# Kernel tuning notes

Measured on AMD Instinct MI355X. Metric: run time of the kernel, lower is better.

The kernel has to match this reference:

```python
import jax, jax.numpy as jnp
import numpy as np

N = 100000
E = 3200000
IN_FEATS = 128
HID_FEATS = 128
OUT_FEATS = 128
MLP_HID = 128
MLP_OUT = 64


def setup_inputs() -> dict:
    key = jax.random.key(0)
    ks = jax.random.split(key, 12)
    x = jax.random.normal(ks[0], (N, IN_FEATS), dtype=jnp.float32)
    src = jax.random.randint(ks[1], (E,), 0, N, dtype=jnp.int32)
    dst = jax.random.randint(ks[2], (E,), 0, N, dtype=jnp.int32)
    s = 0.05
    W1 = jax.random.normal(ks[3], (IN_FEATS, HID_FEATS), dtype=jnp.float32) * s
    b1 = jnp.zeros((HID_FEATS,), dtype=jnp.float32)
    W2 = jax.random.normal(ks[4], (HID_FEATS, OUT_FEATS), dtype=jnp.float32) * s
    b2 = jnp.zeros((OUT_FEATS,), dtype=jnp.float32)
    Wm1 = jax.random.normal(ks[5], (OUT_FEATS, MLP_HID), dtype=jnp.float32) * s
    bm1 = jnp.zeros((MLP_HID,), dtype=jnp.float32)
    Wm2 = jax.random.normal(ks[6], (MLP_HID, MLP_OUT), dtype=jnp.float32) * s
    bm2 = jnp.zeros((MLP_OUT,), dtype=jnp.float32)
    return {"x": x, "src": src, "dst": dst, "W1": W1, "b1": b1,
            "W2": W2, "b2": b2, "Wm1": Wm1, "bm1": bm1, "Wm2": Wm2, "bm2": bm2}


def _graph_conv(h, src, dst, W, b, out_norm, in_norm):
    # DGL GraphConv norm='both': rst = D_in^{-1/2} * A^T (D_out^{-1/2} * h) @ W + b
    msg = (h * out_norm[:, None])[src]                       # [E, F] gather
    agg = jax.ops.segment_sum(msg, dst, num_segments=N)      # [N, F] scatter-add
    return (agg * in_norm[:, None]) @ W + b


def _forward(x, src, dst, W1, b1, W2, b2, Wm1, bm1, Wm2, bm2):
    ones = jnp.ones((src.shape[0],), dtype=x.dtype)
    out_deg = jnp.maximum(jax.ops.segment_sum(ones, src, num_segments=N), 1.0)
    in_deg = jnp.maximum(jax.ops.segment_sum(ones, dst, num_segments=N), 1.0)
    out_norm = out_deg ** -0.5
    in_norm = in_deg ** -0.5
    # conv1 + ReLU (dropout identity in eval mode)
    h = jax.nn.relu(_graph_conv(x, src, dst, W1, b1, out_norm, in_norm))
    # conv2 + ReLU
    h = jax.nn.relu(_graph_conv(h, src, dst, W2, b2, out_norm, in_norm))
    # MLP head: Linear -> ReLU -> Linear -> sigmoid (act='sigmoid')
    h = jax.nn.relu(h @ Wm1 + bm1)
    h = jax.nn.sigmoid(h @ Wm2 + bm2)
    return h


def reference(x, src, dst, W1, b1, W2, b2, Wm1, bm1, Wm2, bm2):
    return _forward(x, src, dst, W1, b1, W2, b2, Wm1, bm1, Wm2, bm2)
```

## Files before the change

### kernel.cpp

```cpp
#include <hip/hip_runtime.h>
#include <math.h>

#define NNODES 100000
#define NEDGES 3200000
#define F 128
#define NPB 512
#define NB ((NNODES + NPB - 1) / NPB)
#define CAP 20480
#define T2 8192

typedef __attribute__((ext_vector_type(8))) short short8;
typedef __attribute__((ext_vector_type(4))) float f32x4;

__device__ __forceinline__ unsigned short f2bf(float f) {
    unsigned u = __float_as_uint(f);
    unsigned r = u + 0x7fff + ((u >> 16) & 1);
    return (unsigned short)(r >> 16);
}
__device__ __forceinline__ float bflo(unsigned u) { return __uint_as_float(u << 16); }
__device__ __forceinline__ float bfhi(unsigned u) { return __uint_as_float(u & 0xffff0000u); }


__global__ void init_cursors_kernel(int* __restrict__ dcur, int* __restrict__ scur) {
    int b = blockIdx.x * 256 + threadIdx.x;
    if (b < NB) { dcur[b] = b * CAP; scur[b] = b * CAP; }
}


__global__ __launch_bounds__(256) void dual_bin_kernel(const int* __restrict__ src,
                                                       const int* __restrict__ dst,
                                                       int* __restrict__ dcur,
                                                       int* __restrict__ scur,
                                                       unsigned* __restrict__ epk,
                                                       unsigned short* __restrict__ esl) {
    __shared__ unsigned pk[T2];
    __shared__ unsigned short sl[T2];
    __shared__ unsigned char db[T2], sb[T2];
    __shared__ int dh[NB], dbase[NB], dlc[NB];
    __shared__ int sh[NB], sbase[NB], slc[NB];
    int t = threadIdx.x;
    for (int i = t; i < NB; i += 256) { dh[i] = 0; dlc[i] = 0; sh[i] = 0; slc[i] = 0; }
    __syncthreads();
    int e0 = blockIdx.x * T2;
    int n = min(T2, NEDGES - e0);
    for (int i = t; i < n; i += 256) {
        int s = src[e0 + i], d = dst[e0 + i];
        int bd = d >> 9, bs = s >> 9;
        pk[i] = (unsigned)s | ((unsigned)(d & 511) << 17);
        sl[i] = (unsigned short)(s & 511);
        db[i] = (unsigned char)bd;
        sb[i] = (unsigned char)bs;
        atomicAdd(&dh[bd], 1);
        atomicAdd(&sh[bs], 1);
    }
    __syncthreads();
    for (int b = t; b < NB; b += 256) {
        if (dh[b]) dbase[b] = atomicAdd(&dcur[b], dh[b]);
        if (sh[b]) sbase[b] = atomicAdd(&scur[b], sh[b]);
    }
    __syncthreads();
    for (int i = t; i < n; i += 256) {
        int b = db[i];
        epk[dbase[b] + atomicAdd(&dlc[b], 1)] = pk[i];
    }
    for (int i = t; i < n; i += 256) {
        int b = sb[i];
        esl[sbase[b] + atomicAdd(&slc[b], 1)] = sl[i];
    }
}


__global__ __launch_bounds__(512) void src_hist_kernel(const unsigned short* __restrict__ esl,
                                                       const int* __restrict__ scur,
                                                       float* __restrict__ out_norm) {
    __shared__ int cnt[NPB];
    int t = threadIdx.x, b = blockIdx.x;
    cnt[t] = 0;
    __syncthreads();
    int e0 = b * CAP, e1 = scur[b];
    for (int i = e0 + t; i < e1; i += 512) atomicAdd(&cnt[esl[i]], 1);
    __syncthreads();
    int node = b * NPB + t;
    if (node < NNODES) out_norm[node] = rsqrtf((float)max(cnt[t], 1));
}


__global__ __launch_bounds__(512) void bucket_csr_kernel(const unsigned* __restrict__ epk,
                                                         const int* __restrict__ dcur,
                                                         int2* __restrict__ row_span,
                                                         float* __restrict__ in_norm,
                                                         int* __restrict__ csr_src) {
    __shared__ int hist[NPB], off[NPB], lcur[NPB];
    int t = threadIdx.x, b = blockIdx.x;
    hist[t] = 0; lcur[t] = 0;
    __syncthreads();
    int e0 = b * CAP, e1 = dcur[b];
    for (int i = e0 + t; i < e1; i += 512)
        atomicAdd(&hist[epk[i] >> 17], 1);
    __syncthreads();
    int h = hist[t];
    off[t] = h;
    __syncthreads();
    for (int d = 1; d < NPB; d <<= 1) {
        int u = (t >= d) ? off[t - d] : 0;
        __syncthreads();
        off[t] += u;
        __syncthreads();
    }
    int excl = off[t] - h;
    int node = b * NPB + t;
    if (node < NNODES) {
        row_span[node] = make_int2(e0 + excl, e0 + excl + h);
        in_norm[node] = rsqrtf((float)max(h, 1));
    }
    __syncthreads();
    off[t] = excl;
    __syncthreads();
    for (int i = e0 + t; i < e1; i += 512) {
        unsigned p = epk[i];
        int dl = p >> 17;
        csr_src[e0 + off[dl] + atomicAdd(&lcur[dl], 1)] = (int)(p & 0x1FFFF);
    }
}


__global__ __launch_bounds__(256) void scale_to_bf16_kernel(const float* __restrict__ x,
                                                            const float* __restrict__ out_norm,
                                                            uint2* __restrict__ hs) {
    int tid = blockIdx.x * 256 + threadIdx.x;
    if (tid >= NNODES * 32) return;
    int row = tid >> 5, q = tid & 31;
    float nrm = out_norm[row];
    float4 v = *(const float4*)(x + (size_t)row * F + q * 4);
    uint2 o;
    o.x = (unsigned)f2bf(v.x * nrm) | ((unsigned)f2bf(v.y * nrm) << 16);
    o.y = (unsigned)f2bf(v.z * nrm) | ((unsigned)f2bf(v.w * nrm) << 16);
    hs[(size_t)row * 32 + q] = o;
}


__global__ void pack_all_kernel(const float* __restrict__ W1, const float* __restrict__ W2,
                                const float* __restrict__ Wm1, const float* __restrict__ Wm2,
                                short8* __restrict__ Wp) {
    int idx = blockIdx.x * 256 + threadIdx.x;
    if (idx >= 7168) return;
    const float* W; int ncol, base;
    if (idx < 2048)      { W = W1;  ncol = 128; base = 0; }
    else if (idx < 4096) { W = W2;  ncol = 128; base = 2048; }
    else if (idx < 6144) { W = Wm1; ncol = 128; base = 4096; }
    else                 { W = Wm2; ncol = 64;  base = 6144; }
    int li = idx - base;
    int lane = li & 63, s = (li >> 6) & 3, c = li >> 8;
    int nn = c * 16 + (lane & 15);
    int k0 = s * 32 + (lane >> 4) * 8;
    short8 v;
#pragma unroll
    for (int j = 0; j < 8; j++) v[j] = (short)f2bf(W[(size_t)(k0 + j) * ncol + nn]);
    Wp[idx] = v;
}


__global__ __launch_bounds__(256) void aggregate_kernel(const unsigned* __restrict__ hs,
                                                        const int2* __restrict__ row_span,
                                                        const int* __restrict__ csr_src,
                                                        const float* __restrict__ in_norm,
                                                        unsigned* __restrict__ outv) {
    int wave = threadIdx.x >> 6;
    int lane = threadIdx.x & 63;
    int node = blockIdx.x * 4 + wave;
    if (node >= NNODES) return;
    int2 sp = row_span[node];
    int beg = sp.x, end = sp.y;
    float ax = 0.f, ay = 0.f;
    int j = beg;
    for (; j + 8 <= end; j += 8) {
        int s0 = csr_src[j],     s1 = csr_src[j + 1], s2 = csr_src[j + 2], s3 = csr_src[j + 3];
        int s4 = csr_src[j + 4], s5 = csr_src[j + 5], s6 = csr_src[j + 6], s7 = csr_src[j + 7];
        unsigned u0 = hs[(size_t)s0 * 64 + lane];
        unsigned u1 = hs[(size_t)s1 * 64 + lane];
        unsigned u2 = hs[(size_t)s2 * 64 + lane];
        unsigned u3 = hs[(size_t)s3 * 64 + lane];
        unsigned u4 = hs[(size_t)s4 * 64 + lane];
        unsigned u5 = hs[(size_t)s5 * 64 + lane];
        unsigned u6 = hs[(size_t)s6 * 64 + lane];
        unsigned u7 = hs[(size_t)s7 * 64 + lane];
        ax += bflo(u0) + bflo(u1) + bflo(u2) + bflo(u3)
            + bflo(u4) + bflo(u5) + bflo(u6) + bflo(u7);
        ay += bfhi(u0) + bfhi(u1) + bfhi(u2) + bfhi(u3)
            + bfhi(u4) + bfhi(u5) + bfhi(u6) + bfhi(u7);
    }
    for (; j < end; j++) {
        unsigned u0 = hs[(size_t)csr_src[j] * 64 + lane];
        ax += bflo(u0);
        ay += bfhi(u0);
    }
    float inn = in_norm[node];
    outv[(size_t)node * 64 + lane] =
        (unsigned)f2bf(ax * inn) | ((unsigned)f2bf(ay * inn) << 16);
}


template <int SCALE>
__global__ __launch_bounds__(256) void gemm_mfma_kernel(const unsigned short* __restrict__ A,
                                                        const short8* __restrict__ Bp,
                                                        const float* __restrict__ bias,
                                                        const float* __restrict__ out_norm,
                                                        unsigned short* __restrict__ Cout, int nrows) {
    int w = threadIdx.x >> 6, lane = threadIdx.x & 63;
    int m = lane & 15, quad = lane >> 4;
    int row0 = blockIdx.x * 64 + w * 16;

    int arow = min(row0 + m, nrows - 1);
    short8 afrag[4];
#pragma unroll
    for (int s = 0; s < 4; s++)
        afrag[s] = *(const short8*)(A + (size_t)arow * F + s * 32 + quad * 8);

    int baseRow = row0 + quad * 4;
    float nrm[4];
    if (SCALE) {
#pragma unroll
        for (int r = 0; r < 4; r++) nrm[r] = out_norm[min(baseRow + r, nrows - 1)];
    }

#pragma unroll
    for (int c = 0; c < 8; c++) {
        f32x4 acc = {0.f, 0.f, 0.f, 0.f};
#pragma unroll
        for (int s = 0; s < 4; s++) {
            short8 b = Bp[(c * 4 + s) * 64 + lane];
            acc = __builtin_amdgcn_mfma_f32_16x16x32_bf16(afrag[s], b, acc, 0, 0, 0);
        }
        float bc = bias[c * 16 + m];
#pragma unroll
        for (int r = 0; r < 4; r++) {
            int row = baseRow + r;
            if (row < nrows) {
                float v = fmaxf(acc[r] + bc, 0.f);
                if (SCALE) v *= nrm[r];
                Cout[(size_t)row * F + c * 16 + m] = f2bf(v);
            }
        }
    }
}


__global__ __launch_bounds__(256) void mlp_fused_kernel(const unsigned short* __restrict__ A,
                                                        const short8* __restrict__ Bp1,
                                                        const float* __restrict__ bm1,
                                                        const short8* __restrict__ Bp2,
                                                        const float* __restrict__ bm2,
                                                        float* __restrict__ out, int nrows) {
    __shared__ unsigned short h3[4][16][136];
    int w = threadIdx.x >> 6, lane = threadIdx.x & 63;
    int m = lane & 15, quad = lane >> 4;
    int row0 = blockIdx.x * 64 + w * 16;

    int arow = min(row0 + m, nrows - 1);
    short8 afrag[4];
#pragma unroll
    for (int s = 0; s < 4; s++)
        afrag[s] = *(const short8*)(A + (size_t)arow * F + s * 32 + quad * 8);

#pragma unroll
    for (int c = 0; c < 8; c++) {
        f32x4 acc = {0.f, 0.f, 0.f, 0.f};
#pragma unroll
        for (int s = 0; s < 4; s++) {
            short8 b = Bp1[(c * 4 + s) * 64 + lane];
            acc = __builtin_amdgcn_mfma_f32_16x16x32_bf16(afrag[s], b, acc, 0, 0, 0);
        }
        float bc = bm1[c * 16 + m];
#pragma unroll
        for (int r = 0; r < 4; r++)
            h3[w][quad * 4 + r][c * 16 + m] = f2bf(fmaxf(acc[r] + bc, 0.f));
    }
    __syncthreads();

    short8 a2[4];
#pragma unroll
    for (int s = 0; s < 4; s++)
        a2[s] = *(const short8*)(&h3[w][m][s * 32 + quad * 8]);

    int baseRow = row0 + quad * 4;
#pragma unroll
    for (int c2 = 0; c2 < 4; c2++) {
        f32x4 acc = {0.f, 0.f, 0.f, 0.f};
#pragma unroll
        for (int s = 0; s < 4; s++) {
            short8 b = Bp2[(c2 * 4 + s) * 64 + lane];
            acc = __builtin_amdgcn_mfma_f32_16x16x32_bf16(a2[s], b, acc, 0, 0, 0);
        }
        float bc = bm2[c2 * 16 + m];
#pragma unroll
        for (int r = 0; r < 4; r++) {
            int row = baseRow + r;
            if (row < nrows)
                out[(size_t)row * 64 + c2 * 16 + m] = 1.f / (1.f + __expf(-(acc[r] + bc)));
        }
    }
}


extern "C" void kernel_launch(void* const* d_in, const int* in_sizes, int n_in,
                              void* d_out, int out_size, void* d_ws, size_t ws_size,
                              hipStream_t stream) {
    const float* x   = (const float*)d_in[0];
    const int* src   = (const int*)d_in[1];
    const int* dst   = (const int*)d_in[2];
    const float* W1  = (const float*)d_in[3];
    const float* b1  = (const float*)d_in[4];
    const float* W2  = (const float*)d_in[5];
    const float* b2  = (const float*)d_in[6];
    const float* Wm1 = (const float*)d_in[7];
    const float* bm1 = (const float*)d_in[8];
    const float* Wm2 = (const float*)d_in[9];
    const float* bm2 = (const float*)d_in[10];
    float* out = (float*)d_out;

    char* w = (char*)d_ws;
    int* dcur          = (int*)w;   w += (size_t)(NB + 4) * 4;
    int* scur          = (int*)w;   w += (size_t)(NB + 4) * 4;
    float* out_norm    = (float*)w; w += (size_t)NNODES * 4;
    float* in_norm     = (float*)w; w += (size_t)NNODES * 4;
    int2* row_span     = (int2*)w;  w += (size_t)NNODES * 8;
    int* csr_src       = (int*)w;   w += (size_t)NB * CAP * 4;
    unsigned* epk      = (unsigned*)w; w += (size_t)NB * CAP * 4;
    unsigned short* esl= (unsigned short*)w; w += (size_t)NB * CAP * 2;
    short8* Wp         = (short8*)w; w += (size_t)7168 * 16;
    unsigned* bufX     = (unsigned*)w; w += (size_t)NNODES * 64 * 4;
    unsigned* bufY     = (unsigned*)w; w += (size_t)NNODES * 64 * 4;

    init_cursors_kernel<<<1, 256, 0, stream>>>(dcur, scur);
    dual_bin_kernel<<<(NEDGES + T2 - 1) / T2, 256, 0, stream>>>(src, dst, dcur, scur, epk, esl);
    src_hist_kernel<<<NB, 512, 0, stream>>>(esl, scur, out_norm);
    bucket_csr_kernel<<<NB, 512, 0, stream>>>(epk, dcur, row_span, in_norm, csr_src);
    scale_to_bf16_kernel<<<(NNODES * 32 + 255) / 256, 256, 0, stream>>>(x, out_norm, (uint2*)bufX);
    pack_all_kernel<<<28, 256, 0, stream>>>(W1, W2, Wm1, Wm2, Wp);

    const int aggGrid = (NNODES + 3) / 4;
    const int gemmGrid = (NNODES + 63) / 64;

    aggregate_kernel<<<aggGrid, 256, 0, stream>>>(bufX, row_span, csr_src, in_norm, bufY);
    gemm_mfma_kernel<1><<<gemmGrid, 256, 0, stream>>>((const unsigned short*)bufY, Wp, b1, out_norm,
                                                      (unsigned short*)bufX, NNODES);
    aggregate_kernel<<<aggGrid, 256, 0, stream>>>(bufX, row_span, csr_src, in_norm, bufY);
    gemm_mfma_kernel<0><<<gemmGrid, 256, 0, stream>>>((const unsigned short*)bufY, Wp + 2048, b2, out_norm,
                                                      (unsigned short*)bufX, NNODES);
    mlp_fused_kernel<<<gemmGrid, 256, 0, stream>>>((const unsigned short*)bufX, Wp + 4096, bm1,
                                                   Wp + 6144, bm2, out, NNODES);
}
```

Before: 566.8 us.

## Slice node features into column-major feature slices for cache-local gather aggregation

Stores bf16 node features as 8 feature slices of 16 columns each (slice-major) instead of row-major, and splits aggregation across blocks by slice so that each slice's working set (about 3.2MB) fits better in cache during random gathers. Each half-wave handles one node, with 8 edge groups processing 4 uint2 lanes per edge, followed by a shuffle reduction. The GEMM and MLP kernels are updated to read and write the sliced layout. In exchange, the CSR index reads are repeated once per slice and each gather is only 32 bytes, which may hurt memory coalescing.

```diff
diff --git a/kernel.cpp b/kernel.cpp
--- a/kernel.cpp
+++ b/kernel.cpp
@@ -8,6 +8,7 @@
 #define NB ((NNODES + NPB - 1) / NPB)
 #define CAP 20480
 #define T2 8192
+#define NSLICE 8
 
 typedef __attribute__((ext_vector_type(8))) short short8;
 typedef __attribute__((ext_vector_type(4))) float f32x4;
@@ -135,7 +136,7 @@
     uint2 o;
     o.x = (unsigned)f2bf(v.x * nrm) | ((unsigned)f2bf(v.y * nrm) << 16);
     o.y = (unsigned)f2bf(v.z * nrm) | ((unsigned)f2bf(v.w * nrm) << 16);
-    hs[(size_t)row * 32 + q] = o;
+    hs[((size_t)(q >> 2) * NNODES + row) * 4 + (q & 3)] = o;
 }
 
 
@@ -160,43 +161,56 @@
 }
 
 
-__global__ __launch_bounds__(256) void aggregate_kernel(const unsigned* __restrict__ hs,
+__global__ __launch_bounds__(256) void aggregate_kernel(const uint2* __restrict__ hsv,
                                                         const int2* __restrict__ row_span,
                                                         const int* __restrict__ csr_src,
                                                         const float* __restrict__ in_norm,
-                                                        unsigned* __restrict__ outv) {
+                                                        uint2* __restrict__ outv) {
+    int slice = blockIdx.x & 7;
+    int grp = blockIdx.x >> 3;
+    int lane = threadIdx.x & 63;
     int wave = threadIdx.x >> 6;
-    int lane = threadIdx.x & 63;
-    int node = blockIdx.x * 4 + wave;
-    if (node >= NNODES) return;
+    int half = lane >> 5;
+    int node = grp * 8 + wave * 2 + half;
+    int g  = (lane & 31) >> 2;
+    int ql = lane & 3;
     int2 sp = row_span[node];
     int beg = sp.x, end = sp.y;
-    float ax = 0.f, ay = 0.f;
-    int j = beg;
-    for (; j + 8 <= end; j += 8) {
-        int s0 = csr_src[j],     s1 = csr_src[j + 1], s2 = csr_src[j + 2], s3 = csr_src[j + 3];
-        int s4 = csr_src[j + 4], s5 = csr_src[j + 5], s6 = csr_src[j + 6], s7 = csr_src[j + 7];
-        unsigned u0 = hs[(size_t)s0 * 64 + lane];
-        unsigned u1 = hs[(size_t)s1 * 64 + lane];
-        unsigned u2 = hs[(size_t)s2 * 64 + lane];
-        unsigned u3 = hs[(size_t)s3 * 64 + lane];
-        unsigned u4 = hs[(size_t)s4 * 64 + lane];
-        unsigned u5 = hs[(size_t)s5 * 64 + lane];
-        unsigned u6 = hs[(size_t)s6 * 64 + lane];
-        unsigned u7 = hs[(size_t)s7 * 64 + lane];
-        ax += bflo(u0) + bflo(u1) + bflo(u2) + bflo(u3)
-            + bflo(u4) + bflo(u5) + bflo(u6) + bflo(u7);
-        ay += bfhi(u0) + bfhi(u1) + bfhi(u2) + bfhi(u3)
-            + bfhi(u4) + bfhi(u5) + bfhi(u6) + bfhi(u7);
-    }
-    for (; j < end; j++) {
-        unsigned u0 = hs[(size_t)csr_src[j] * 64 + lane];
-        ax += bflo(u0);
-        ay += bfhi(u0);
-    }
+    const uint2* base = hsv + (size_t)slice * (NNODES * 4);
+    float a0 = 0.f, a1 = 0.f, a2 = 0.f, a3 = 0.f;
+    int myK = (end - beg + 7) >> 3;
+    int oK  = __shfl_xor(myK, 32);
+    int kmax = (myK > oK) ? myK : oK;
+    int lim = end - 1; if (lim < 0) lim = 0;
+    for (int k = 0; k < kmax; k += 2) {
+        int e0 = beg + k * 8 + g;
+        int e1 = e0 + 8;
+        int i0 = min(e0, lim);
+        int i1 = min(e1, lim);
+        int r0 = csr_src[i0];
+        int r1 = csr_src[i1];
+        uint2 u0 = base[(size_t)r0 * 4 + ql];
+        uint2 u1 = base[(size_t)r1 * 4 + ql];
+        if (e0 >= end) { u0.x = 0u; u0.y = 0u; }
+        if (e1 >= end) { u1.x = 0u; u1.y = 0u; }
+        a0 += bflo(u0.x) + bflo(u1.x);
+        a1 += bfhi(u0.x) + bfhi(u1.x);
+        a2 += bflo(u0.y) + bflo(u1.y);
+        a3 += bfhi(u0.y) + bfhi(u1.y);
+    }
+    a0 += __shfl_xor(a0, 4);  a1 += __shfl_xor(a1, 4);
+    a2 += __shfl_xor(a2, 4);  a3 += __shfl_xor(a3, 4);
+    a0 += __shfl_xor(a0, 8);  a1 += __shfl_xor(a1, 8);
+    a2 += __shfl_xor(a2, 8);  a3 += __shfl_xor(a3, 8);
+    a0 += __shfl_xor(a0, 16); a1 += __shfl_xor(a1, 16);
+    a2 += __shfl_xor(a2, 16); a3 += __shfl_xor(a3, 16);
     float inn = in_norm[node];
-    outv[(size_t)node * 64 + lane] =
-        (unsigned)f2bf(ax * inn) | ((unsigned)f2bf(ay * inn) << 16);
+    if ((lane & 31) < 4) {
+        uint2 o;
+        o.x = (unsigned)f2bf(a0 * inn) | ((unsigned)f2bf(a1 * inn) << 16);
+        o.y = (unsigned)f2bf(a2 * inn) | ((unsigned)f2bf(a3 * inn) << 16);
+        outv[((size_t)slice * NNODES + node) * 4 + ql] = o;
+    }
 }
 
 
@@ -214,7 +228,7 @@
     short8 afrag[4];
 #pragma unroll
     for (int s = 0; s < 4; s++)
-        afrag[s] = *(const short8*)(A + (size_t)arow * F + s * 32 + quad * 8);
+        afrag[s] = *(const short8*)(A + ((size_t)(2 * s + (quad >> 1)) * NNODES + arow) * 16 + (quad & 1) * 8);
 
     int baseRow = row0 + quad * 4;
     float nrm[4];
@@ -238,7 +252,7 @@
             if (row < nrows) {
                 float v = fmaxf(acc[r] + bc, 0.f);
                 if (SCALE) v *= nrm[r];
-                Cout[(size_t)row * F + c * 16 + m] = f2bf(v);
+                Cout[((size_t)c * NNODES + row) * 16 + m] = f2bf(v);
             }
         }
     }
@@ -260,7 +274,7 @@
     short8 afrag[4];
 #pragma unroll
     for (int s = 0; s < 4; s++)
-        afrag[s] = *(const short8*)(A + (size_t)arow * F + s * 32 + quad * 8);
+        afrag[s] = *(const short8*)(A + ((size_t)(2 * s + (quad >> 1)) * NNODES + arow) * 16 + (quad & 1) * 8);
 
 #pragma unroll
     for (int c = 0; c < 8; c++) {
@@ -338,13 +352,13 @@
     scale_to_bf16_kernel<<<(NNODES * 32 + 255) / 256, 256, 0, stream>>>(x, out_norm, (uint2*)bufX);
     pack_all_kernel<<<28, 256, 0, stream>>>(W1, W2, Wm1, Wm2, Wp);
 
-    const int aggGrid = (NNODES + 3) / 4;
+    const int aggGrid = (NNODES / 8) * NSLICE;
     const int gemmGrid = (NNODES + 63) / 64;
 
-    aggregate_kernel<<<aggGrid, 256, 0, stream>>>(bufX, row_span, csr_src, in_norm, bufY);
+    aggregate_kernel<<<aggGrid, 256, 0, stream>>>((const uint2*)bufX, row_span, csr_src, in_norm, (uint2*)bufY);
     gemm_mfma_kernel<1><<<gemmGrid, 256, 0, stream>>>((const unsigned short*)bufY, Wp, b1, out_norm,
                                                       (unsigned short*)bufX, NNODES);
-    aggregate_kernel<<<aggGrid, 256, 0, stream>>>(bufX, row_span, csr_src, in_norm, bufY);
+    aggregate_kernel<<<aggGrid, 256, 0, stream>>>(bufX ? (const uint2*)bufX : nullptr, row_span, csr_src, in_norm, (uint2*)bufY);
     gemm_mfma_kernel<0><<<gemmGrid, 256, 0, stream>>>((const unsigned short*)bufY, Wp + 2048, b2, out_norm,
                                                       (unsigned short*)bufX, NNODES);
     mlp_fused_kernel<<<gemmGrid, 256, 0, stream>>>((const unsigned short*)bufX, Wp + 4096, bm1,
```

Measured after the change: 584.6 us. 1.03x slower.

## Slice feature matrix into 16-column panels and aggregate one node per thread

Applied to the files above, without the earlier changes.

Stores node features in a sliced layout: 8 panels of 16 bf16 columns, each holding all nodes contiguously. Aggregation now assigns one thread per node per slice and gathers 32-byte chunks, so each slice's working set (about 3.2 MB) can stay in cache. This replaces the old scheme of one wave per node reading 256-byte rows. The GEMM and MLP kernels are changed to read and write the same layout. The cost is that each thread walks its whole edge list serially, so lanes with different degrees diverge and every slice re-reads the CSR indices.

```diff
diff --git a/kernel.cpp b/kernel.cpp
--- a/kernel.cpp
+++ b/kernel.cpp
@@ -8,9 +8,11 @@
 #define NB ((NNODES + NPB - 1) / NPB)
 #define CAP 20480
 #define T2 8192
+#define NSLICE 8
 
 typedef __attribute__((ext_vector_type(8))) short short8;
 typedef __attribute__((ext_vector_type(4))) float f32x4;
+typedef __attribute__((ext_vector_type(4))) unsigned uintx4;
 
 __device__ __forceinline__ unsigned short f2bf(float f) {
     unsigned u = __float_as_uint(f);
@@ -135,7 +137,7 @@
     uint2 o;
     o.x = (unsigned)f2bf(v.x * nrm) | ((unsigned)f2bf(v.y * nrm) << 16);
     o.y = (unsigned)f2bf(v.z * nrm) | ((unsigned)f2bf(v.w * nrm) << 16);
-    hs[(size_t)row * 32 + q] = o;
+    hs[((size_t)(q >> 2) * NNODES + row) * 4 + (q & 3)] = o;
 }
 
 
@@ -160,43 +162,44 @@
 }
 
 
-__global__ __launch_bounds__(256) void aggregate_kernel(const unsigned* __restrict__ hs,
+__global__ __launch_bounds__(256) void aggregate_kernel(const uintx4* __restrict__ hsv4,
                                                         const int2* __restrict__ row_span,
                                                         const int* __restrict__ csr_src,
                                                         const float* __restrict__ in_norm,
-                                                        unsigned* __restrict__ outv) {
-    int wave = threadIdx.x >> 6;
-    int lane = threadIdx.x & 63;
-    int node = blockIdx.x * 4 + wave;
+                                                        uintx4* __restrict__ outv4) {
+    int slice = blockIdx.x & 7;
+    int node = (blockIdx.x >> 3) * 256 + threadIdx.x;
     if (node >= NNODES) return;
+    const uintx4* base = hsv4 + (size_t)slice * (NNODES * 2);
     int2 sp = row_span[node];
-    int beg = sp.x, end = sp.y;
-    float ax = 0.f, ay = 0.f;
-    int j = beg;
-    for (; j + 8 <= end; j += 8) {
-        int s0 = csr_src[j],     s1 = csr_src[j + 1], s2 = csr_src[j + 2], s3 = csr_src[j + 3];
-        int s4 = csr_src[j + 4], s5 = csr_src[j + 5], s6 = csr_src[j + 6], s7 = csr_src[j + 7];
-        unsigned u0 = hs[(size_t)s0 * 64 + lane];
-        unsigned u1 = hs[(size_t)s1 * 64 + lane];
-        unsigned u2 = hs[(size_t)s2 * 64 + lane];
-        unsigned u3 = hs[(size_t)s3 * 64 + lane];
-        unsigned u4 = hs[(size_t)s4 * 64 + lane];
-        unsigned u5 = hs[(size_t)s5 * 64 + lane];
-        unsigned u6 = hs[(size_t)s6 * 64 + lane];
-        unsigned u7 = hs[(size_t)s7 * 64 + lane];
-        ax += bflo(u0) + bflo(u1) + bflo(u2) + bflo(u3)
-            + bflo(u4) + bflo(u5) + bflo(u6) + bflo(u7);
-        ay += bfhi(u0) + bfhi(u1) + bfhi(u2) + bfhi(u3)
-            + bfhi(u4) + bfhi(u5) + bfhi(u6) + bfhi(u7);
-    }
-    for (; j < end; j++) {
-        unsigned u0 = hs[(size_t)csr_src[j] * 64 + lane];
-        ax += bflo(u0);
-        ay += bfhi(u0);
+    float s0 = 0.f, s1 = 0.f, s2 = 0.f, s3 = 0.f, s4 = 0.f, s5 = 0.f, s6 = 0.f, s7 = 0.f,
+          s8 = 0.f, s9 = 0.f, s10 = 0.f, s11 = 0.f, s12 = 0.f, s13 = 0.f, s14 = 0.f, s15 = 0.f;
+    for (int e = sp.x; e < sp.y; ++e) {
+        unsigned r = (unsigned)__builtin_nontemporal_load(csr_src + e);
+        uintx4 a = hsv4[(size_t)slice * (NNODES * 2) + (size_t)r * 2];
+        uintx4 b = base[(size_t)r * 2 + 1];
+        s0 += bflo(a.x);  s1 += bfhi(a.x);
+        s2 += bflo(a.y);  s3 += bfhi(a.y);
+        s4 += bflo(a.z);  s5 += bfhi(a.z);
+        s6 += bflo(a.w);  s7 += bfhi(a.w);
+        s8 += bflo(b.x);  s9 += bfhi(b.x);
+        s10 += bflo(b.y); s11 += bfhi(b.y);
+        s12 += bflo(b.z); s13 += bfhi(b.z);
+        s14 += bflo(b.w); s15 += bfhi(b.w);
     }
     float inn = in_norm[node];
-    outv[(size_t)node * 64 + lane] =
-        (unsigned)f2bf(ax * inn) | ((unsigned)f2bf(ay * inn) << 16);
+    uintx4 o0, o1;
+    o0.x = (unsigned)f2bf(s0 * inn)  | ((unsigned)f2bf(s1 * inn) << 16);
+    o0.y = (unsigned)f2bf(s2 * inn)  | ((unsigned)f2bf(s3 * inn) << 16);
+    o0.z = (unsigned)f2bf(s4 * inn)  | ((unsigned)f2bf(s5 * inn) << 16);
+    o0.w = (unsigned)f2bf(s6 * inn)  | ((unsigned)f2bf(s7 * inn) << 16);
+    o1.x = (unsigned)f2bf(s8 * inn)  | ((unsigned)f2bf(s9 * inn) << 16);
+    o1.y = (unsigned)f2bf(s10 * inn) | ((unsigned)f2bf(s11 * inn) << 16);
+    o1.z = (unsigned)f2bf(s12 * inn) | ((unsigned)f2bf(s13 * inn) << 16);
+    o1.w = (unsigned)f2bf(s14 * inn) | ((unsigned)f2bf(s15 * inn) << 16);
+    size_t ob = ((size_t)slice * NNODES + node) * 2;
+    __builtin_nontemporal_store(o0, outv4 + ob);
+    __builtin_nontemporal_store(o1, outv4 + ob + 1);
 }
 
 
@@ -214,7 +217,7 @@
     short8 afrag[4];
 #pragma unroll
     for (int s = 0; s < 4; s++)
-        afrag[s] = *(const short8*)(A + (size_t)arow * F + s * 32 + quad * 8);
+        afrag[s] = *(const short8*)(A + ((size_t)(2 * s + (quad >> 1)) * NNODES + arow) * 16 + (quad & 1) * 8);
 
     int baseRow = row0 + quad * 4;
     float nrm[4];
@@ -238,7 +241,7 @@
             if (row < nrows) {
                 float v = fmaxf(acc[r] + bc, 0.f);
                 if (SCALE) v *= nrm[r];
-                Cout[(size_t)row * F + c * 16 + m] = f2bf(v);
+                Cout[((size_t)c * NNODES + row) * 16 + m] = f2bf(v);
             }
         }
     }
@@ -260,7 +263,7 @@
     short8 afrag[4];
 #pragma unroll
     for (int s = 0; s < 4; s++)
-        afrag[s] = *(const short8*)(A + (size_t)arow * F + s * 32 + quad * 8);
+        afrag[s] = *(const short8*)(A + ((size_t)(2 * s + (quad >> 1)) * NNODES + arow) * 16 + (quad & 1) * 8);
 
 #pragma unroll
     for (int c = 0; c < 8; c++) {
@@ -338,13 +341,13 @@
     scale_to_bf16_kernel<<<(NNODES * 32 + 255) / 256, 256, 0, stream>>>(x, out_norm, (uint2*)bufX);
     pack_all_kernel<<<28, 256, 0, stream>>>(W1, W2, Wm1, Wm2, Wp);
 
-    const int aggGrid = (NNODES + 3) / 4;
+    const int aggGrid = ((NNODES + 255) / 256) * NSLICE;
     const int gemmGrid = (NNODES + 63) / 64;
 
-    aggregate_kernel<<<aggGrid, 256, 0, stream>>>(bufX, row_span, csr_src, in_norm, bufY);
+    aggregate_kernel<<<aggGrid, 256, 0, stream>>>((const uintx4*)bufX, row_span, csr_src, in_norm, (uintx4*)bufY);
     gemm_mfma_kernel<1><<<gemmGrid, 256, 0, stream>>>((const unsigned short*)bufY, Wp, b1, out_norm,
                                                       (unsigned short*)bufX, NNODES);
-    aggregate_kernel<<<aggGrid, 256, 0, stream>>>(bufX, row_span, csr_src, in_norm, bufY);
+    aggregate_kernel<<<aggGrid, 256, 0, stream>>>((const uintx4*)bufX, row_span, csr_src, in_norm, (uintx4*)bufY);
     gemm_mfma_kernel<0><<<gemmGrid, 256, 0, stream>>>((const unsigned short*)bufY, Wp + 2048, b2, out_norm,
                                                       (unsigned short*)bufX, NNODES);
     mlp_fused_kernel<<<gemmGrid, 256, 0, stream>>>((const unsigned short*)bufX, Wp + 4096, bm1,
```

Measured after the change: 1.397 ms. 146% more time.

## Slice node features into 8 column blocks to shrink aggregation gather working set

Applied to the files above, without the earlier changes.

Node feature buffers move from row-major [N][128] bf16 to eight feature slices of [N][16] bf16, and the aggregate, scale, GEMM and MLP kernels are rewritten to index this layout. Each aggregate block now handles one slice for 32 nodes, with 8 lanes per node, so every gather reads 32 bytes from a 3.2 MB slice. The aim is to keep each slice's working set cached during the random gathers instead of streaming the full feature matrix. In exchange each gather is a small segment, CSR indices are read eight times, and the GEMM A loads are less contiguous. Grid sizing assumes NNODES divides by 32.

```diff
diff --git a/kernel.cpp b/kernel.cpp
--- a/kernel.cpp
+++ b/kernel.cpp
@@ -8,6 +8,7 @@
 #define NB ((NNODES + NPB - 1) / NPB)
 #define CAP 20480
 #define T2 8192
+#define NSLICE 8
 
 typedef __attribute__((ext_vector_type(8))) short short8;
 typedef __attribute__((ext_vector_type(4))) float f32x4;
@@ -135,7 +136,7 @@
     uint2 o;
     o.x = (unsigned)f2bf(v.x * nrm) | ((unsigned)f2bf(v.y * nrm) << 16);
     o.y = (unsigned)f2bf(v.z * nrm) | ((unsigned)f2bf(v.w * nrm) << 16);
-    hs[(size_t)row * 32 + q] = o;
+    hs[((size_t)(q >> 2) * NNODES + row) * 4 + (q & 3)] = o;
 }
 
 
@@ -160,43 +161,37 @@
 }
 
 
-__global__ __launch_bounds__(256) void aggregate_kernel(const unsigned* __restrict__ hs,
+__global__ __launch_bounds__(256) void aggregate_kernel(const unsigned* __restrict__ hsu,
                                                         const int2* __restrict__ row_span,
                                                         const int* __restrict__ csr_src,
                                                         const float* __restrict__ in_norm,
-                                                        unsigned* __restrict__ outv) {
+                                                        unsigned* __restrict__ outu) {
+    int slice = blockIdx.x & 7;
     int wave = threadIdx.x >> 6;
     int lane = threadIdx.x & 63;
-    int node = blockIdx.x * 4 + wave;
-    if (node >= NNODES) return;
+    int sub  = lane >> 3;
+    int fp   = lane & 7;
+    int node = (blockIdx.x >> 3) * 32 + wave * 8 + sub;
+    const unsigned* base = hsu + (size_t)slice * ((size_t)NNODES * 8);
     int2 sp = row_span[node];
-    int beg = sp.x, end = sp.y;
-    float ax = 0.f, ay = 0.f;
-    int j = beg;
-    for (; j + 8 <= end; j += 8) {
-        int s0 = csr_src[j],     s1 = csr_src[j + 1], s2 = csr_src[j + 2], s3 = csr_src[j + 3];
-        int s4 = csr_src[j + 4], s5 = csr_src[j + 5], s6 = csr_src[j + 6], s7 = csr_src[j + 7];
-        unsigned u0 = hs[(size_t)s0 * 64 + lane];
-        unsigned u1 = hs[(size_t)s1 * 64 + lane];
-        unsigned u2 = hs[(size_t)s2 * 64 + lane];
-        unsigned u3 = hs[(size_t)s3 * 64 + lane];
-        unsigned u4 = hs[(size_t)s4 * 64 + lane];
-        unsigned u5 = hs[(size_t)s5 * 64 + lane];
-        unsigned u6 = hs[(size_t)s6 * 64 + lane];
-        unsigned u7 = hs[(size_t)s7 * 64 + lane];
-        ax += bflo(u0) + bflo(u1) + bflo(u2) + bflo(u3)
-            + bflo(u4) + bflo(u5) + bflo(u6) + bflo(u7);
-        ay += bfhi(u0) + bfhi(u1) + bfhi(u2) + bfhi(u3)
-            + bfhi(u4) + bfhi(u5) + bfhi(u6) + bfhi(u7);
-    }
-    for (; j < end; j++) {
-        unsigned u0 = hs[(size_t)csr_src[j] * 64 + lane];
-        ax += bflo(u0);
-        ay += bfhi(u0);
+    int e = sp.x, end = sp.y;
+    float sx = 0.f, sy = 0.f;
+    for (; e + 1 < end; e += 2) {
+        unsigned r0 = (unsigned)csr_src[e];
+        unsigned r1 = (unsigned)csr_src[e + 1];
+        unsigned v0 = base[(r0 << 3) | fp];
+        unsigned v1 = base[(r1 << 3) | fp];
+        sx += bflo(v0) + bflo(v1);
+        sy += bfhi(v0) + bfhi(v1);
+    }
+    if (e < end) {
+        unsigned v = base[((unsigned)csr_src[e] << 3) | fp];
+        sx += bflo(v);
+        sy += bfhi(v);
     }
     float inn = in_norm[node];
-    outv[(size_t)node * 64 + lane] =
-        (unsigned)f2bf(ax * inn) | ((unsigned)f2bf(ay * inn) << 16);
+    unsigned o = (unsigned)f2bf(sx * inn) | ((unsigned)f2bf(sy * inn) << 16);
+    __builtin_nontemporal_store(o, outu + ((size_t)slice * NNODES + node) * 8 + fp);
 }
 
 
@@ -214,7 +209,7 @@
     short8 afrag[4];
 #pragma unroll
     for (int s = 0; s < 4; s++)
-        afrag[s] = *(const short8*)(A + (size_t)arow * F + s * 32 + quad * 8);
+        afrag[s] = *(const short8*)(A + ((size_t)(2 * s + (quad >> 1)) * NNODES + arow) * 16 + (quad & 1) * 8);
 
     int baseRow = row0 + quad * 4;
     float nrm[4];
@@ -238,7 +233,7 @@
             if (row < nrows) {
                 float v = fmaxf(acc[r] + bc, 0.f);
                 if (SCALE) v *= nrm[r];
-                Cout[(size_t)row * F + c * 16 + m] = f2bf(v);
+                Cout[((size_t)c * NNODES + row) * 16 + m] = f2bf(v);
             }
         }
     }
@@ -260,7 +255,7 @@
     short8 afrag[4];
 #pragma unroll
     for (int s = 0; s < 4; s++)
-        afrag[s] = *(const short8*)(A + (size_t)arow * F + s * 32 + quad * 8);
+        afrag[s] = *(const short8*)(A + ((size_t)(2 * s + (quad >> 1)) * NNODES + arow) * 16 + (quad & 1) * 8);
 
 #pragma unroll
     for (int c = 0; c < 8; c++) {
@@ -338,7 +333,7 @@
     scale_to_bf16_kernel<<<(NNODES * 32 + 255) / 256, 256, 0, stream>>>(x, out_norm, (uint2*)bufX);
     pack_all_kernel<<<28, 256, 0, stream>>>(W1, W2, Wm1, Wm2, Wp);
 
-    const int aggGrid = (NNODES + 3) / 4;
+    const int aggGrid = (NNODES / 32) * NSLICE;
     const int gemmGrid = (NNODES + 63) / 64;
 
     aggregate_kernel<<<aggGrid, 256, 0, stream>>>(bufX, row_span, csr_src, in_norm, bufY);
```

Measured after the change: 674.8 us. 19.1% more time.
